# Performance work log

Measured on AMD Instinct MI355X. Metric: run time of the kernel, lower is better.

Reference implementation:

```python
import jax, jax.numpy as jnp
import numpy as np

TEMPERATURE = 0.07
NEG_INF = -1e30


def setup_inputs() -> dict:
    key = jax.random.key(0)
    k_h, k_m, k_l, k_w = jax.random.split(key, 4)
    B, L, H, P = 32, 1024, 1280, 128
    hidden_states = jax.random.normal(k_h, (B, L, H), dtype=jnp.float32)
    attention_mask = jax.random.randint(k_m, (B, L), 0, 2).astype(jnp.int32)
    labels = jax.random.randint(k_l, (B, L), 0, 4).astype(jnp.int32)
    proj_w = jax.random.normal(k_w, (H, P), dtype=jnp.float32) * 0.02
    proj_b = jnp.zeros((P,), dtype=jnp.float32)
    return {
        "hidden_states": hidden_states,
        "proj_w": proj_w,
        "proj_b": proj_b,
        "attention_mask": attention_mask,
        "labels": labels,
    }


def reference(hidden_states, proj_w, proj_b, attention_mask, labels):
    # Projection head (dropout is inactive at eval) + L2 normalize
    emb = hidden_states @ proj_w + proj_b                     # [B, L, P]
    emb = emb / jnp.linalg.norm(emb, axis=-1, keepdims=True)

    B, L, _ = emb.shape
    attn_valid = attention_mask.astype(bool)                  # [B, L]
    valid = attn_valid & (labels != -100)                     # anchor/candidate validity

    # Per-sequence token-token similarity, temperature-scaled
    sim = jnp.einsum("bip,bjp->bij", emb, emb) / TEMPERATURE  # [B, L, L]

    eye = jnp.eye(L, dtype=bool)                              # [L, L]
    col_valid = valid[:, None, :]                             # valid candidate j
    # Row max over valid columns (includes self, as in original filtered emb)
    m = jax.lax.stop_gradient(
        jnp.max(jnp.where(col_valid, sim, NEG_INF), axis=2, keepdims=True)
    )
    logits = sim - m
    logits_mask = col_valid & ~eye[None]                      # exclude self, invalid cols
    exp_logits = jnp.where(logits_mask, jnp.exp(logits), 0.0)
    log_prob = logits - jnp.log(exp_logits.sum(axis=2, keepdims=True) + 1e-12)

    # Positives: same label, same sequence, not self, both valid
    same_label = labels[:, :, None] == labels[:, None, :]
    pos_mask = (same_label & logits_mask & valid[:, :, None]).astype(sim.dtype)

    sum_pos_log_prob = (pos_mask * log_prob).sum(axis=2)      # [B, L]
    anchor_loss = sum_pos_log_prob / (pos_mask.sum(axis=2) + 1e-12)

    valid_f = valid.astype(sim.dtype)
    n_anchor = jnp.maximum(valid_f.sum(axis=1), 1.0)
    loss_seq = -(valid_f * anchor_loss).sum(axis=1) / n_anchor  # mean over valid anchors

    # Sequence included iff attention_mask has >= 2 valid tokens (original check)
    seq_ok = (attention_mask.sum(axis=1) >= 2)
    n_seq = jnp.maximum(seq_ok.sum().astype(sim.dtype), 1.0)
    loss = jnp.where(seq_ok, loss_seq, 0.0).sum() / n_seq
    return loss
```

## Files before the change

### kernel.cpp

```cpp
#include <hip/hip_runtime.h>
#include <hip/hip_bf16.h>
#include <cstddef>
#include <cstdint>

#define NB   32
#define LSEQ 1024
#define HDIM 1280
#define PDIM 128
#define KSTEPS 20

typedef unsigned short ushort_t;
typedef __bf16 bf16x8 __attribute__((ext_vector_type(8)));
typedef float  f32x4  __attribute__((ext_vector_type(4)));

#define WT_OFF  256
#define E_OFF   (256 + HDIM * PDIM * 2)

__device__ __forceinline__ ushort_t bf16_rne(float x) {
  unsigned u = __float_as_uint(x);
  unsigned r = u + 0x7fffu + ((u >> 16) & 1u);
  return (ushort_t)(r >> 16);
}

#define GLD_LDS16(gp, lp)                                                      \
  __builtin_amdgcn_global_load_lds(                                            \
      (const __attribute__((address_space(1))) void*)(gp),                     \
      (__attribute__((address_space(3))) void*)(lp), 16, 0, 0)

__global__ __launch_bounds__(256) void k0_wt(const float* __restrict__ pw,
                                             ushort_t* __restrict__ wB,
                                             float* __restrict__ wsf) {
  if (blockIdx.x == 0 && threadIdx.x < 64) wsf[threadIdx.x] = 0.0f;
  const int idx = blockIdx.x * 256 + threadIdx.x;
  const int k = idx >> 7, n = idx & 127;
  const int kc = k >> 5, kr = k & 31;
  const int t = n >> 4, lm = n & 15;
  const int lq = kr >> 3, j = kr & 7;
  const int l = lq * 16 + lm;
  wB[((size_t)(kc * 8 + t) * 64 + l) * 8 + j] = bf16_rne(pw[(size_t)k * PDIM + n]);
}

__global__ __launch_bounds__(256, 4) void k1_mfma(const float* __restrict__ hs,
                                                  const ushort_t* __restrict__ wB,
                                                  const float* __restrict__ pb,
                                                  ushort_t* __restrict__ e) {
  __shared__ __align__(16) char smem[2][8192];

  const int tid = threadIdx.x;
  const int l = tid & 63, w = tid >> 6;
  const int lm = l & 15, lq = l >> 4;
  const int m0 = blockIdx.x * 32;

  const int o0 = w * 1024 + l * 16;
  const int o1 = o0 + 4096;
  const float* ga0;
  const float* ga1;
  {
    int p = o0 >> 10;
    int row = ((p >> 2) << 4) + lm;
    int kk  = (((p >> 1) & 1) << 5) + (lq << 3) + ((p & 1) << 2);
    ga0 = hs + (size_t)(m0 + row) * HDIM + kk;
    p = o1 >> 10;
    row = ((p >> 2) << 4) + lm;
    kk  = (((p >> 1) & 1) << 5) + (lq << 3) + ((p & 1) << 2);
    ga1 = hs + (size_t)(m0 + row) * HDIM + kk;
  }
  const ushort_t* bB = wB + (size_t)(w * 2) * 512 + (size_t)l * 8;

  f32x4 acc[2][2];
#pragma unroll
  for (int m = 0; m < 2; ++m)
#pragma unroll
    for (int tt = 0; tt < 2; ++tt) acc[m][tt] = (f32x4){0.f, 0.f, 0.f, 0.f};

  GLD_LDS16(ga0, &smem[0][o0]);
  GLD_LDS16(ga1, &smem[0][o1]);
  ga0 += 64; ga1 += 64;
  __syncthreads();

#pragma unroll 2
  for (int st = 0; st < KSTEPS; ++st) {
    const int cur = st & 1;

    bf16x8 Bf[2][2];
#pragma unroll
    for (int kh = 0; kh < 2; ++kh)
#pragma unroll
      for (int tt = 0; tt < 2; ++tt)
        Bf[tt][kh] =
            *(const bf16x8*)(bB + (size_t)(st * 2 + kh) * 4096 + tt * 512);

    if (st < KSTEPS - 1) {
      GLD_LDS16(ga0, &smem[cur ^ 1][o0]);
      GLD_LDS16(ga1, &smem[cur ^ 1][o1]);
      ga0 += 64; ga1 += 64;
    }

    bf16x8 a[2][2];
#pragma unroll
    for (int m = 0; m < 2; ++m)
#pragma unroll
      for (int kh = 0; kh < 2; ++kh) {
        const f32x4 f0 =
            *(const f32x4*)&smem[cur][(m * 4 + kh * 2 + 0) * 1024 + l * 16];
        const f32x4 f1 =
            *(const f32x4*)&smem[cur][(m * 4 + kh * 2 + 1) * 1024 + l * 16];
        union { ushort_t u[8]; bf16x8 v; } cv;
        cv.u[0] = bf16_rne(f0[0]); cv.u[1] = bf16_rne(f0[1]);
        cv.u[2] = bf16_rne(f0[2]); cv.u[3] = bf16_rne(f0[3]);
        cv.u[4] = bf16_rne(f1[0]); cv.u[5] = bf16_rne(f1[1]);
        cv.u[6] = bf16_rne(f1[2]); cv.u[7] = bf16_rne(f1[3]);
        a[m][kh] = cv.v;
      }

#pragma unroll
    for (int m = 0; m < 2; ++m)
#pragma unroll
      for (int tt = 0; tt < 2; ++tt)
#pragma unroll
        for (int kh = 0; kh < 2; ++kh)
          acc[m][tt] = __builtin_amdgcn_mfma_f32_16x16x32_bf16(
              a[m][kh], Bf[tt][kh], acc[m][tt], 0, 0, 0);

    __syncthreads();
  }

  const float pbv0 = pb[w * 32 + lm];
  const float pbv1 = pb[w * 32 + 16 + lm];
#pragma unroll
  for (int m = 0; m < 2; ++m)
#pragma unroll
    for (int r = 0; r < 4; ++r) {
      acc[m][0][r] += pbv0;
      acc[m][1][r] += pbv1;
    }

  float* sp = (float*)smem;
#pragma unroll
  for (int m = 0; m < 2; ++m)
#pragma unroll
    for (int r = 0; r < 4; ++r) {
      float s2 = acc[m][0][r] * acc[m][0][r] + acc[m][1][r] * acc[m][1][r];
      s2 += __shfl_xor(s2, 1, 64);
      s2 += __shfl_xor(s2, 2, 64);
      s2 += __shfl_xor(s2, 4, 64);
      s2 += __shfl_xor(s2, 8, 64);
      if (lm == 0) sp[w * 32 + m * 16 + lq * 4 + r] = s2;
    }
  __syncthreads();

#pragma unroll
  for (int m = 0; m < 2; ++m)
#pragma unroll
    for (int r = 0; r < 4; ++r) {
      const int row = m * 16 + lq * 4 + r;
      const float tot = sp[row] + sp[32 + row] + sp[64 + row] + sp[96 + row];
      const float inv = 1.0f / sqrtf(tot);
      ushort_t* er = e + (size_t)(m0 + row) * PDIM + w * 32 + lm;
      er[0]  = bf16_rne(acc[m][0][r] * inv);
      er[16] = bf16_rne(acc[m][1][r] * inv);
    }
}

__global__ __launch_bounds__(256, 3) void k2_loss(const ushort_t* __restrict__ e,
                                                  const int* __restrict__ mask,
                                                  const int* __restrict__ labels,
                                                  float* __restrict__ accb) {
  __shared__ float part[4][32][3];

  const int tid = threadIdx.x;
  const int l = tid & 63, w = tid >> 6;
  const int b  = blockIdx.x >> 5;
  const int i0 = (blockIdx.x & 31) << 5;
  const int lm = l & 15, lq = l >> 4;

  const ushort_t* eb   = e + (size_t)b * LSEQ * PDIM;
  const int*      mrow = mask + b * LSEQ;
  const int*      lrow = labels + b * LSEQ;

  bf16x8 af[2][4];
#pragma unroll
  for (int ii = 0; ii < 2; ++ii) {
    const ushort_t* aptr = eb + (size_t)(i0 + ii * 16 + lm) * PDIM + lq * 8;
#pragma unroll
    for (int c = 0; c < 4; ++c) af[ii][c] = *(const bf16x8*)(aptr + c * 32);
  }

  int  li[2][4], ar[2][4];
  bool vi[2][4];
#pragma unroll
  for (int ii = 0; ii < 2; ++ii)
#pragma unroll
    for (int r = 0; r < 4; ++r) {
      ar[ii][r] = i0 + ii * 16 + lq * 4 + r;
      li[ii][r] = lrow[ar[ii][r]];
      vi[ii][r] = (mrow[ar[ii][r]] != 0) && (li[ii][r] != -100);
    }

  float d[2][4] = {}, ps[2][4] = {}, pc[2][4] = {};
  const float invT = 1.0f / 0.07f;

  int jt = w * 16;
  bf16x8 Bc[4];
  int ljc, mjc;
  {
    const int j = jt * 16 + lm;
    const ushort_t* bptr = eb + (size_t)j * PDIM + lq * 8;
#pragma unroll
    for (int c = 0; c < 4; ++c) Bc[c] = *(const bf16x8*)(bptr + c * 32);
    ljc = lrow[j];
    mjc = mrow[j];
  }

#pragma unroll 1
  for (int s = 0; s < 16; ++s, ++jt) {
    bf16x8 Bn[4];
    int ljn = 0, mjn = 0;
    if (s < 15) {
      const int jn = (jt + 1) * 16 + lm;
      const ushort_t* bptr = eb + (size_t)jn * PDIM + lq * 8;
#pragma unroll
      for (int c = 0; c < 4; ++c) Bn[c] = *(const bf16x8*)(bptr + c * 32);
      ljn = lrow[jn];
      mjn = mrow[jn];
    }

    const int j = jt * 16 + lm;
    const bool cvj = (mjc != 0) && (ljc != -100);
#pragma unroll
    for (int ii = 0; ii < 2; ++ii) {
      f32x4 acc = (f32x4){0.f, 0.f, 0.f, 0.f};
#pragma unroll
      for (int c = 0; c < 4; ++c)
        acc = __builtin_amdgcn_mfma_f32_16x16x32_bf16(af[ii][c], Bc[c], acc, 0, 0, 0);
#pragma unroll
      for (int r = 0; r < 4; ++r) {
        const float sv = acc[r] * invT;
        const bool dm  = cvj && (j != ar[ii][r]);
        const float ex = __expf(sv);
        d[ii][r] += dm ? ex : 0.f;
        const bool pos = dm && (ljc == li[ii][r]) && vi[ii][r];
        ps[ii][r] += pos ? sv : 0.f;
        pc[ii][r] += pos ? 1.f : 0.f;
      }
    }

#pragma unroll
    for (int c = 0; c < 4; ++c) Bc[c] = Bn[c];
    ljc = ljn; mjc = mjn;
  }

#pragma unroll
  for (int ii = 0; ii < 2; ++ii)
#pragma unroll
    for (int r = 0; r < 4; ++r) {
#pragma unroll
      for (int off = 1; off < 16; off <<= 1) {
        d[ii][r]  += __shfl_xor(d[ii][r], off, 64);
        ps[ii][r] += __shfl_xor(ps[ii][r], off, 64);
        pc[ii][r] += __shfl_xor(pc[ii][r], off, 64);
      }
    }
  if (lm == 0) {
#pragma unroll
    for (int ii = 0; ii < 2; ++ii)
#pragma unroll
      for (int r = 0; r < 4; ++r) {
        part[w][ii * 16 + lq * 4 + r][0] = d[ii][r];
        part[w][ii * 16 + lq * 4 + r][1] = ps[ii][r];
        part[w][ii * 16 + lq * 4 + r][2] = pc[ii][r];
      }
  }
  __syncthreads();

  if (tid < 32) {
    float D = 0.f, P = 0.f, C = 0.f;
#pragma unroll
    for (int w2 = 0; w2 < 4; ++w2) {
      D += part[w2][tid][0];
      P += part[w2][tid][1];
      C += part[w2][tid][2];
    }
    const float logD = logf(D + 1e-12f);
    float al = (P - C * logD) / (C + 1e-12f);
#pragma unroll
    for (int off = 1; off < 32; off <<= 1) al += __shfl_xor(al, off, 64);
    if (tid == 0) atomicAdd(&accb[b], al);
  }
}

__global__ __launch_bounds__(1024) void k3_final(const int* __restrict__ mask,
                                                 const int* __restrict__ labels,
                                                 const float* __restrict__ accb,
                                                 float* __restrict__ out) {
  __shared__ float lossv[NB];
  __shared__ float okv[NB];
  const int t = threadIdx.x;
  const int b = t >> 5, sub = t & 31;

  int cm = 0, cv = 0;
#pragma unroll
  for (int q = 0; q < 8; ++q) {
    const int idx = b * LSEQ + q * 128 + sub * 4;
    const int4 mv = *(const int4*)(mask + idx);
    const int4 lv = *(const int4*)(labels + idx);
    cm += mv.x + mv.y + mv.z + mv.w;
    cv += ((mv.x != 0 && lv.x != -100) ? 1 : 0) +
          ((mv.y != 0 && lv.y != -100) ? 1 : 0) +
          ((mv.z != 0 && lv.z != -100) ? 1 : 0) +
          ((mv.w != 0 && lv.w != -100) ? 1 : 0);
  }
#pragma unroll
  for (int off = 16; off; off >>= 1) {
    cm += __shfl_xor(cm, off, 64);
    cv += __shfl_xor(cv, off, 64);
  }
  if (sub == 0) {
    const bool ok = (cm >= 2);
    lossv[b] = ok ? (-accb[b] / fmaxf((float)cv, 1.0f)) : 0.0f;
    okv[b]   = ok ? 1.0f : 0.0f;
  }
  __syncthreads();
  if (t < NB) {
    float lv = lossv[t], ov = okv[t];
#pragma unroll
    for (int off = 16; off; off >>= 1) {
      lv += __shfl_xor(lv, off, 64);
      ov += __shfl_xor(ov, off, 64);
    }
    if (t == 0) out[0] = lv / fmaxf(ov, 1.0f);
  }
}

extern "C" void kernel_launch(void* const* d_in, const int* in_sizes, int n_in,
                              void* d_out, int out_size, void* d_ws, size_t ws_size,
                              hipStream_t stream) {
  (void)in_sizes; (void)n_in; (void)out_size; (void)ws_size;
  const float* hs     = (const float*)d_in[0];
  const float* pw     = (const float*)d_in[1];
  const float* pb     = (const float*)d_in[2];
  const int*   mask   = (const int*)d_in[3];
  const int*   labels = (const int*)d_in[4];
  float* out = (float*)d_out;

  char* wsb = (char*)d_ws;
  float*    wsf  = (float*)wsb;
  float*    accb = wsf;
  ushort_t* wB   = (ushort_t*)(wsb + WT_OFF);
  ushort_t* e    = (ushort_t*)(wsb + E_OFF);

  k0_wt<<<(HDIM * PDIM) / 256, 256, 0, stream>>>(pw, wB, wsf);
  k1_mfma<<<(NB * LSEQ) / 32, 256, 0, stream>>>(hs, wB, pb, e);
  k2_loss<<<NB * 32, 256, 0, stream>>>(e, mask, labels, accb);
  k3_final<<<1, 1024, 0, stream>>>(mask, labels, accb, out);
}
```

Before: 299.8 us.

## Deepen projection GEMM pipeline to 4-stage LDS ring with swizzled row layout

The projection kernel moves from a double-buffered LDS staging of the hidden-state tiles to a four-buffer ring that prefetches three k-steps ahead. Explicit vmcnt waits plus a barrier replace __syncthreads. The global loads now fetch contiguous row segments into an XOR-swizzled LDS layout, which should improve coalescing and reduce bank conflicts. Weight fragments are register-prefetched one step ahead. This aims to hide HBM latency in a memory-bound GEMM, at the cost of more LDS per block and hand-tuned wait counts that must match the number of outstanding loads.

```diff
diff --git a/kernel.cpp b/kernel.cpp
--- a/kernel.cpp
+++ b/kernel.cpp
@@ -26,6 +26,9 @@
   __builtin_amdgcn_global_load_lds(                                            \
       (const __attribute__((address_space(1))) void*)(gp),                     \
       (__attribute__((address_space(3))) void*)(lp), 16, 0, 0)
+
+#define WAIT_BAR(N)                                                            \
+  asm volatile("s_waitcnt vmcnt(" #N ") lgkmcnt(0)\n\ts_barrier" ::: "memory")
 
 __global__ __launch_bounds__(256) void k0_wt(const float* __restrict__ pw,
                                              ushort_t* __restrict__ wB,
@@ -44,27 +47,20 @@
                                                   const ushort_t* __restrict__ wB,
                                                   const float* __restrict__ pb,
                                                   ushort_t* __restrict__ e) {
-  __shared__ __align__(16) char smem[2][8192];
+  __shared__ __align__(16) char smem[4][8192];
 
   const int tid = threadIdx.x;
   const int l = tid & 63, w = tid >> 6;
   const int lm = l & 15, lq = l >> 4;
   const int m0 = blockIdx.x * 32;
 
-  const int o0 = w * 1024 + l * 16;
-  const int o1 = o0 + 4096;
-  const float* ga0;
-  const float* ga1;
-  {
-    int p = o0 >> 10;
-    int row = ((p >> 2) << 4) + lm;
-    int kk  = (((p >> 1) & 1) << 5) + (lq << 3) + ((p & 1) << 2);
-    ga0 = hs + (size_t)(m0 + row) * HDIM + kk;
-    p = o1 >> 10;
-    row = ((p >> 2) << 4) + lm;
-    kk  = (((p >> 1) & 1) << 5) + (lq << 3) + ((p & 1) << 2);
-    ga1 = hs + (size_t)(m0 + row) * HDIM + kk;
-  }
+  const int r0 = tid >> 4;
+  const int cp = tid & 15;
+  const int cs = cp ^ (r0 & 7);
+  const float* ga0 = hs + (size_t)(m0 + r0) * HDIM + cs * 4;
+  const float* ga1 = ga0 + (size_t)16 * HDIM;
+  const int d0 = tid * 16, d1 = 4096 + tid * 16;
+
   const ushort_t* bB = wB + (size_t)(w * 2) * 512 + (size_t)l * 8;
 
   f32x4 acc[2][2];
@@ -73,38 +69,49 @@
 #pragma unroll
     for (int tt = 0; tt < 2; ++tt) acc[m][tt] = (f32x4){0.f, 0.f, 0.f, 0.f};
 
-  GLD_LDS16(ga0, &smem[0][o0]);
-  GLD_LDS16(ga1, &smem[0][o1]);
-  ga0 += 64; ga1 += 64;
-  __syncthreads();
-
-#pragma unroll 2
+  GLD_LDS16(ga0 + 0,   &smem[0][d0]); GLD_LDS16(ga1 + 0,   &smem[0][d1]);
+  GLD_LDS16(ga0 + 64,  &smem[1][d0]); GLD_LDS16(ga1 + 64,  &smem[1][d1]);
+  GLD_LDS16(ga0 + 128, &smem[2][d0]); GLD_LDS16(ga1 + 128, &smem[2][d1]);
+
+  bf16x8 Bc[2][2], Bn[2][2];
+#pragma unroll
+  for (int kh = 0; kh < 2; ++kh)
+#pragma unroll
+    for (int tt = 0; tt < 2; ++tt)
+      Bc[tt][kh] = *(const bf16x8*)(bB + (size_t)kh * 4096 + tt * 512);
+
+#pragma unroll
   for (int st = 0; st < KSTEPS; ++st) {
-    const int cur = st & 1;
-
-    bf16x8 Bf[2][2];
-#pragma unroll
-    for (int kh = 0; kh < 2; ++kh)
-#pragma unroll
-      for (int tt = 0; tt < 2; ++tt)
-        Bf[tt][kh] =
-            *(const bf16x8*)(bB + (size_t)(st * 2 + kh) * 4096 + tt * 512);
+    if (st == 0)                 WAIT_BAR(0);
+    else if (st == 1)            WAIT_BAR(4);
+    else if (st >= KSTEPS - 2)   WAIT_BAR(8);
+    else                         WAIT_BAR(12);
+
+    if (st < KSTEPS - 3) {
+      GLD_LDS16(ga0 + (st + 3) * 64, &smem[(st + 3) & 3][d0]);
+      GLD_LDS16(ga1 + (st + 3) * 64, &smem[(st + 3) & 3][d1]);
+    }
 
     if (st < KSTEPS - 1) {
-      GLD_LDS16(ga0, &smem[cur ^ 1][o0]);
-      GLD_LDS16(ga1, &smem[cur ^ 1][o1]);
-      ga0 += 64; ga1 += 64;
-    }
-
+#pragma unroll
+      for (int kh = 0; kh < 2; ++kh)
+#pragma unroll
+        for (int tt = 0; tt < 2; ++tt)
+          Bn[tt][kh] = *(const bf16x8*)(bB + (size_t)((st + 1) * 2 + kh) * 4096 +
+                                        tt * 512);
+    }
+
+    const char* buf = smem[st & 3];
     bf16x8 a[2][2];
 #pragma unroll
     for (int m = 0; m < 2; ++m)
 #pragma unroll
       for (int kh = 0; kh < 2; ++kh) {
-        const f32x4 f0 =
-            *(const f32x4*)&smem[cur][(m * 4 + kh * 2 + 0) * 1024 + l * 16];
-        const f32x4 f1 =
-            *(const f32x4*)&smem[cur][(m * 4 + kh * 2 + 1) * 1024 + l * 16];
+        const int base = (m * 16 + lm) * 256;
+        const int c0 = ((kh * 8 + lq * 2 + 0) ^ (lm & 7)) * 16;
+        const int c1 = ((kh * 8 + lq * 2 + 1) ^ (lm & 7)) * 16;
+        const f32x4 f0 = *(const f32x4*)&buf[base + c0];
+        const f32x4 f1 = *(const f32x4*)&buf[base + c1];
         union { ushort_t u[8]; bf16x8 v; } cv;
         cv.u[0] = bf16_rne(f0[0]); cv.u[1] = bf16_rne(f0[1]);
         cv.u[2] = bf16_rne(f0[2]); cv.u[3] = bf16_rne(f0[3]);
@@ -120,9 +127,12 @@
 #pragma unroll
         for (int kh = 0; kh < 2; ++kh)
           acc[m][tt] = __builtin_amdgcn_mfma_f32_16x16x32_bf16(
-              a[m][kh], Bf[tt][kh], acc[m][tt], 0, 0, 0);
-
-    __syncthreads();
+              a[m][kh], Bc[tt][kh], acc[m][tt], 0, 0, 0);
+
+#pragma unroll
+    for (int kh = 0; kh < 2; ++kh)
+#pragma unroll
+      for (int tt = 0; tt < 2; ++tt) Bc[tt][kh] = Bn[tt][kh];
   }
 
   const float pbv0 = pb[w * 32 + lm];
```

After: 296.2 us. No clear change (-1.2%).

## Triple-buffer projection GEMM with weights staged through LDS via async loads

Applied to the files above, without the earlier changes.

The projection kernel moves from a double-buffered A-only LDS pipeline to a triple-buffered one where both the hidden-state tile and the bf16 weight tile are fetched with global_load_lds, two stages ahead. Per-stage waits use explicit vmcnt counters with a barrier instead of __syncthreads, so loads can stay in flight across iterations. The A tile layout in LDS changes to a plain row-major arrangement. LDS use per block rises to 72KB and the occupancy hint drops from 4 to 2 blocks, which may reduce latency hiding. The row-major A reads may also cause LDS bank conflicts.

```diff
diff --git a/kernel.cpp b/kernel.cpp
--- a/kernel.cpp
+++ b/kernel.cpp
@@ -26,6 +26,9 @@
   __builtin_amdgcn_global_load_lds(                                            \
       (const __attribute__((address_space(1))) void*)(gp),                     \
       (__attribute__((address_space(3))) void*)(lp), 16, 0, 0)
+
+#define WAIT_BAR(N)                                                            \
+  asm volatile("s_waitcnt vmcnt(" #N ") lgkmcnt(0)\n\ts_barrier" ::: "memory")
 
 __global__ __launch_bounds__(256) void k0_wt(const float* __restrict__ pw,
                                              ushort_t* __restrict__ wB,
@@ -40,32 +43,30 @@
   wB[((size_t)(kc * 8 + t) * 64 + l) * 8 + j] = bf16_rne(pw[(size_t)k * PDIM + n]);
 }
 
-__global__ __launch_bounds__(256, 4) void k1_mfma(const float* __restrict__ hs,
+__global__ __launch_bounds__(256, 2) void k1_mfma(const float* __restrict__ hs,
                                                   const ushort_t* __restrict__ wB,
                                                   const float* __restrict__ pb,
                                                   ushort_t* __restrict__ e) {
-  __shared__ __align__(16) char smem[2][8192];
+  __shared__ __align__(16) char smem[3][24576];
 
   const int tid = threadIdx.x;
   const int l = tid & 63, w = tid >> 6;
   const int lm = l & 15, lq = l >> 4;
   const int m0 = blockIdx.x * 32;
 
-  const int o0 = w * 1024 + l * 16;
-  const int o1 = o0 + 4096;
-  const float* ga0;
-  const float* ga1;
-  {
-    int p = o0 >> 10;
-    int row = ((p >> 2) << 4) + lm;
-    int kk  = (((p >> 1) & 1) << 5) + (lq << 3) + ((p & 1) << 2);
-    ga0 = hs + (size_t)(m0 + row) * HDIM + kk;
-    p = o1 >> 10;
-    row = ((p >> 2) << 4) + lm;
-    kk  = (((p >> 1) & 1) << 5) + (lq << 3) + ((p & 1) << 2);
-    ga1 = hs + (size_t)(m0 + row) * HDIM + kk;
-  }
-  const ushort_t* bB = wB + (size_t)(w * 2) * 512 + (size_t)l * 8;
+  const int ar = tid >> 3, ac = tid & 7;
+  const float* aS = hs + (size_t)(m0 + ar) * HDIM + ac * 4;
+  const char*  bS = (const char*)wB + tid * 16;
+
+#define STAGE(ss, buf)                                                         \
+  do {                                                                         \
+    GLD_LDS16(aS + (ss) * 64,      (buf) + tid * 16);                          \
+    GLD_LDS16(aS + (ss) * 64 + 32, (buf) + 4096 + tid * 16);                   \
+    GLD_LDS16(bS + (size_t)(ss) * 16384,         (buf) + 8192  + tid * 16);    \
+    GLD_LDS16(bS + (size_t)(ss) * 16384 + 4096,  (buf) + 12288 + tid * 16);    \
+    GLD_LDS16(bS + (size_t)(ss) * 16384 + 8192,  (buf) + 16384 + tid * 16);    \
+    GLD_LDS16(bS + (size_t)(ss) * 16384 + 12288, (buf) + 20480 + tid * 16);    \
+  } while (0)
 
   f32x4 acc[2][2];
 #pragma unroll
@@ -73,38 +74,27 @@
 #pragma unroll
     for (int tt = 0; tt < 2; ++tt) acc[m][tt] = (f32x4){0.f, 0.f, 0.f, 0.f};
 
-  GLD_LDS16(ga0, &smem[0][o0]);
-  GLD_LDS16(ga1, &smem[0][o1]);
-  ga0 += 64; ga1 += 64;
-  __syncthreads();
-
-#pragma unroll 2
-  for (int st = 0; st < KSTEPS; ++st) {
-    const int cur = st & 1;
-
-    bf16x8 Bf[2][2];
-#pragma unroll
-    for (int kh = 0; kh < 2; ++kh)
-#pragma unroll
-      for (int tt = 0; tt < 2; ++tt)
-        Bf[tt][kh] =
-            *(const bf16x8*)(bB + (size_t)(st * 2 + kh) * 4096 + tt * 512);
-
-    if (st < KSTEPS - 1) {
-      GLD_LDS16(ga0, &smem[cur ^ 1][o0]);
-      GLD_LDS16(ga1, &smem[cur ^ 1][o1]);
-      ga0 += 64; ga1 += 64;
-    }
+  char* p0 = smem[0];
+  char* p1 = smem[1];
+  char* p2 = smem[2];
+  STAGE(0, p0);
+  STAGE(1, p1);
+
+#pragma unroll 1
+  for (int s = 0; s < KSTEPS; ++s) {
+    if (s < KSTEPS - 1) WAIT_BAR(6);
+    else                WAIT_BAR(0);
+
+    if (s + 2 < KSTEPS) STAGE(s + 2, p2);
 
     bf16x8 a[2][2];
 #pragma unroll
     for (int m = 0; m < 2; ++m)
 #pragma unroll
       for (int kh = 0; kh < 2; ++kh) {
-        const f32x4 f0 =
-            *(const f32x4*)&smem[cur][(m * 4 + kh * 2 + 0) * 1024 + l * 16];
-        const f32x4 f1 =
-            *(const f32x4*)&smem[cur][(m * 4 + kh * 2 + 1) * 1024 + l * 16];
+        const char* base = p0 + kh * 4096 + (m * 16 + lm) * 128 + lq * 32;
+        const f32x4 f0 = *(const f32x4*)base;
+        const f32x4 f1 = *(const f32x4*)(base + 16);
         union { ushort_t u[8]; bf16x8 v; } cv;
         cv.u[0] = bf16_rne(f0[0]); cv.u[1] = bf16_rne(f0[1]);
         cv.u[2] = bf16_rne(f0[2]); cv.u[3] = bf16_rne(f0[3]);
@@ -113,6 +103,14 @@
         a[m][kh] = cv.v;
       }
 
+    bf16x8 Bf[2][2];
+#pragma unroll
+    for (int kh = 0; kh < 2; ++kh)
+#pragma unroll
+      for (int tt = 0; tt < 2; ++tt)
+        Bf[tt][kh] = *(const bf16x8*)(p0 + 8192 +
+                                      ((kh * 8 + w * 2 + tt) * 64 + l) * 16);
+
 #pragma unroll
     for (int m = 0; m < 2; ++m)
 #pragma unroll
@@ -122,8 +120,9 @@
           acc[m][tt] = __builtin_amdgcn_mfma_f32_16x16x32_bf16(
               a[m][kh], Bf[tt][kh], acc[m][tt], 0, 0, 0);
 
-    __syncthreads();
-  }
+    char* tmp = p0; p0 = p1; p1 = p2; p2 = tmp;
+  }
+#undef STAGE
 
   const float pbv0 = pb[w * 32 + lm];
   const float pbv1 = pb[w * 32 + 16 + lm];
```

Measured after the change: 294.5 us. No clear change (-1.8%).
